# Optimization experiments

Hardware: AMD Instinct MI355X
Metric: run time of the kernel (lower is better)

The kernel has to match this reference:

```python
import jax, jax.numpy as jnp
import numpy as np

N, E, C_IN, HID, G, L = 100000, 1600000, 64, 32, 128, 3
NEG_SLOPE = 0.01  # F.leaky_relu default


def setup_inputs() -> dict:
    key = jax.random.key(0)
    ks = jax.random.split(key, 10)
    x = jax.random.normal(ks[0], (N, C_IN), dtype=jnp.float32)
    src = jax.random.randint(ks[1], (E,), 0, N, dtype=jnp.int32)
    dst = jax.random.randint(ks[2], (E,), 0, N, dtype=jnp.int32)
    batch = jnp.sort(jax.random.randint(ks[3], (N,), 0, G, dtype=jnp.int32))
    def glorot(k, fan_in, fan_out):
        lim = np.sqrt(6.0 / (fan_in + fan_out)).astype(np.float32)
        return jax.random.uniform(k, (fan_in, fan_out), jnp.float32, -lim, lim)
    W0 = glorot(ks[4], C_IN, HID); b0 = jnp.zeros((HID,), jnp.float32)
    W1 = glorot(ks[5], HID, HID);  b1 = jnp.zeros((HID,), jnp.float32)
    W2 = glorot(ks[6], HID, HID);  b2 = jnp.zeros((HID,), jnp.float32)
    return {"x": x, "W0": W0, "b0": b0, "W1": W1, "b1": b1,
            "W2": W2, "b2": b2, "src": src, "dst": dst, "batch": batch}


def _gcn_conv(x, W, b, src, dst, dinv):
    # PyG GCNConv: h = x W; aggregate with sym-norm (A + I)
    h = x @ W                                   # [N, H]
    coef = (dinv[src] * dinv[dst])[:, None]     # [E, 1]
    msg = h[src] * coef                         # gather + scale
    agg = jax.ops.segment_sum(msg, dst, num_segments=N)
    agg = agg + h * (dinv * dinv)[:, None]      # self-loop term
    return agg + b


def _mean_pool(x, batch, counts):
    s = jax.ops.segment_sum(x, batch, num_segments=G)
    return s / counts[:, None]


def reference(x, W0, b0, W1, b1, W2, b2, src, dst, batch):
    # degree with self loops (edge weight 1), as PyG gcn_norm does
    deg = jax.ops.segment_sum(jnp.ones((E,), x.dtype), dst, num_segments=N) + 1.0
    dinv = jax.lax.rsqrt(deg)
    counts = jnp.maximum(
        jax.ops.segment_sum(jnp.ones((N,), x.dtype), batch, num_segments=G), 1.0)
    params = [(W0, b0), (W1, b1), (W2, b2)]
    feats = []
    h = x
    for W, b in params:
        h = _gcn_conv(h, W, b, src, dst, dinv)
        h = jax.nn.leaky_relu(h, NEG_SLOPE)
        feats.append(_mean_pool(h, batch, counts))
    merge = jnp.mean(jnp.stack(feats, axis=0), axis=0)  # [G, HID]
    return merge
```

## Files before the change

### kernel.cpp

```cpp
#include <hip/hip_runtime.h>
#include <hip/hip_bf16.h>

#define NN 100000
#define NE 1600000
#define CIN 64
#define HIDN 32
#define NG 128
#define SLOPE 0.01f


__global__ __launch_bounds__(256) void k_rank(const int* __restrict__ dst,
                                              int* __restrict__ deg,
                                              int* __restrict__ rank,
                                              int qbase, int qcount) {
  int i0 = blockIdx.x * 256 + threadIdx.x;
  if (i0 >= qcount) return;
  int i = qbase + i0;
  int4 d = ((const int4*)dst)[i];
  int4 r;
  r.x = atomicAdd(&deg[d.x], 1);
  r.y = atomicAdd(&deg[d.y], 1);
  r.z = atomicAdd(&deg[d.z], 1);
  r.w = atomicAdd(&deg[d.w], 1);
  ((int4*)rank)[i] = r;
}


__global__ __launch_bounds__(256) void k_scan1(const int* __restrict__ deg,
                                               int* __restrict__ bsum) {
  __shared__ int s[256];
  int t = threadIdx.x;
  int base = blockIdx.x * 1024 + t * 4;
  int sum = 0;
#pragma unroll
  for (int j = 0; j < 4; ++j) {
    int idx = base + j;
    if (idx < NN) sum += deg[idx];
  }
  s[t] = sum;
  __syncthreads();
  for (int o = 128; o > 0; o >>= 1) {
    if (t < o) s[t] += s[t + o];
    __syncthreads();
  }
  if (t == 0) bsum[blockIdx.x] = s[0];
}

__global__ __launch_bounds__(256) void k_mid(int* __restrict__ bsum,
                                             int* __restrict__ rowp,
                                             const int* __restrict__ batch,
                                             float* __restrict__ cinv, int nblk) {
  __shared__ int s[128];
  __shared__ int sb[NG + 1];
  int t = threadIdx.x;
  if (t < nblk) s[t] = bsum[t];
  if (t <= NG) {
    int lo = 0, hi = NN;
    while (lo < hi) {
      int mid = (lo + hi) >> 1;
      if (batch[mid] < t) lo = mid + 1; else hi = mid;
    }
    sb[t] = lo;
  }
  __syncthreads();
  if (t == 0) {
    int run = 0;
    for (int i = 0; i < nblk; ++i) {
      int v = s[i];
      s[i] = run;
      run += v;
    }
    rowp[NN] = run;
  }
  __syncthreads();
  if (t < nblk) bsum[t] = s[t];
  if (t < NG) {
    int c = sb[t + 1] - sb[t];
    cinv[t] = 1.0f / (3.0f * fmaxf((float)c, 1.0f));
  }
}

__global__ __launch_bounds__(256) void k_scan3(const int* __restrict__ deg,
                                               const int* __restrict__ bsum,
                                               int* __restrict__ rowp,
                                               float* __restrict__ dinv) {
  __shared__ int s[256];
  int t = threadIdx.x;
  int base = blockIdx.x * 1024 + t * 4;
  int d0 = 0, d1 = 0, d2 = 0, d3 = 0;
  if (base < NN) d0 = deg[base];
  if (base + 1 < NN) d1 = deg[base + 1];
  if (base + 2 < NN) d2 = deg[base + 2];
  if (base + 3 < NN) d3 = deg[base + 3];
  int ts = d0 + d1 + d2 + d3;
  s[t] = ts;
  __syncthreads();
  for (int o = 1; o < 256; o <<= 1) {
    int v = (t >= o) ? s[t - o] : 0;
    __syncthreads();
    s[t] += v;
    __syncthreads();
  }
  int run = bsum[blockIdx.x] + s[t] - ts;
  if (base < NN) { rowp[base] = run; dinv[base] = rsqrtf((float)d0 + 1.0f); run += d0; }
  if (base + 1 < NN) { rowp[base + 1] = run; dinv[base + 1] = rsqrtf((float)d1 + 1.0f); run += d1; }
  if (base + 2 < NN) { rowp[base + 2] = run; dinv[base + 2] = rsqrtf((float)d2 + 1.0f); run += d2; }
  if (base + 3 < NN) { rowp[base + 3] = run; dinv[base + 3] = rsqrtf((float)d3 + 1.0f); run += d3; }
}

__global__ __launch_bounds__(256) void k_scatter(const int* __restrict__ src,
                                                 const int* __restrict__ dst,
                                                 const int* __restrict__ rank,
                                                 const int* __restrict__ rowp,
                                                 int* __restrict__ col,
                                                 int qbase, int qcount) {
  int i0 = blockIdx.x * 256 + threadIdx.x;
  if (i0 >= qcount) return;
  int i = qbase + i0;
  int4 d = ((const int4*)dst)[i];
  int4 r = ((const int4*)rank)[i];
  int4 s = ((const int4*)src)[i];
  col[rowp[d.x] + r.x] = s.x;
  col[rowp[d.y] + r.y] = s.y;
  col[rowp[d.z] + r.z] = s.z;
  col[rowp[d.w] + r.w] = s.w;
}


template <int K>
__global__ __launch_bounds__(256) void k_mm(const float* __restrict__ in,
                                            const float* __restrict__ W,
                                            const float* __restrict__ dinv,
                                            __hip_bfloat16* __restrict__ out) {
  __shared__ float sW[K * HIDN];
  int t = threadIdx.x;
  for (int i = t; i < K * HIDN; i += 256) sW[i] = W[i];
  __syncthreads();
  int gid = blockIdx.x * 256 + t;
  int node = gid >> 5;
  int f = gid & 31;
  if (node >= NN) return;
  const float* xr = in + node * K;
  float acc = 0.f;
#pragma unroll
  for (int k = 0; k < K; ++k) acc += xr[k] * sW[k * HIDN + f];
  out[node * HIDN + f] = __float2bfloat16(acc * dinv[node]);
}


template <int WRITE_H>
__global__ __launch_bounds__(256) void k_agg(const __hip_bfloat16* __restrict__ hs,
                                             const int* __restrict__ rowp,
                                             const int* __restrict__ col,
                                             const float* __restrict__ dinv,
                                             const int* __restrict__ batch,
                                             const float* __restrict__ cinv,
                                             const float* __restrict__ bias,
                                             float* __restrict__ hout,
                                             float* __restrict__ pool) {
  const int t = threadIdx.x;
  const int f = t & 31;
  const int sub = t >> 5;
  const float bf = bias[f];
  float pacc = 0.f;
  int gcur = -1;
  const int base = blockIdx.x * 32;
#pragma unroll
  for (int it = 0; it < 4; ++it) {
    const int i = base + it * 8 + sub;
    if (i < NN) {
      float acc = __bfloat162float(hs[i * HIDN + f]);
      const int rs = rowp[i];
      const int re = rowp[i + 1];
      int e = rs;
      for (; e + 8 <= re; e += 8) {
        const int c0 = __builtin_nontemporal_load(col + e);
        const int c1 = __builtin_nontemporal_load(col + e + 1);
        const int c2 = __builtin_nontemporal_load(col + e + 2);
        const int c3 = __builtin_nontemporal_load(col + e + 3);
        const int c4 = __builtin_nontemporal_load(col + e + 4);
        const int c5 = __builtin_nontemporal_load(col + e + 5);
        const int c6 = __builtin_nontemporal_load(col + e + 6);
        const int c7 = __builtin_nontemporal_load(col + e + 7);
        const float v0 = __bfloat162float(hs[c0 * HIDN + f]);
        const float v1 = __bfloat162float(hs[c1 * HIDN + f]);
        const float v2 = __bfloat162float(hs[c2 * HIDN + f]);
        const float v3 = __bfloat162float(hs[c3 * HIDN + f]);
        const float v4 = __bfloat162float(hs[c4 * HIDN + f]);
        const float v5 = __bfloat162float(hs[c5 * HIDN + f]);
        const float v6 = __bfloat162float(hs[c6 * HIDN + f]);
        const float v7 = __bfloat162float(hs[c7 * HIDN + f]);
        acc += ((v0 + v1) + (v2 + v3)) + ((v4 + v5) + (v6 + v7));
      }
      for (; e + 4 <= re; e += 4) {
        const int c0 = __builtin_nontemporal_load(col + e);
        const int c1 = __builtin_nontemporal_load(col + e + 1);
        const int c2 = __builtin_nontemporal_load(col + e + 2);
        const int c3 = __builtin_nontemporal_load(col + e + 3);
        const float v0 = __bfloat162float(hs[c0 * HIDN + f]);
        const float v1 = __bfloat162float(hs[c1 * HIDN + f]);
        const float v2 = __bfloat162float(hs[c2 * HIDN + f]);
        const float v3 = __bfloat162float(hs[c3 * HIDN + f]);
        acc += (v0 + v1) + (v2 + v3);
      }
      for (; e < re; ++e) acc += __bfloat162float(hs[col[e] * HIDN + f]);
      float v = acc * dinv[i] + bf;
      v = v > 0.f ? v : SLOPE * v;
      if (WRITE_H) hout[i * HIDN + f] = v;
      const int g = batch[i];
      if (g != gcur) {
        if (gcur >= 0) unsafeAtomicAdd(&pool[gcur * HIDN + f], pacc * cinv[gcur]);
        gcur = g;
        pacc = 0.f;
      }
      pacc += v;
    }
  }
  if (gcur >= 0) unsafeAtomicAdd(&pool[gcur * HIDN + f], pacc * cinv[gcur]);
}


extern "C" void kernel_launch(void* const* d_in, const int* in_sizes, int n_in,
                              void* d_out, int out_size, void* d_ws, size_t ws_size,
                              hipStream_t stream) {
  const float* x = (const float*)d_in[0];
  const float* W0 = (const float*)d_in[1];
  const float* b0 = (const float*)d_in[2];
  const float* W1 = (const float*)d_in[3];
  const float* b1 = (const float*)d_in[4];
  const float* W2 = (const float*)d_in[5];
  const float* b2 = (const float*)d_in[6];
  const int* src = (const int*)d_in[7];
  const int* dst = (const int*)d_in[8];
  const int* batch = (const int*)d_in[9];
  float* out = (float*)d_out;

  char* ws = (char*)d_ws;
  auto carve = [&](size_t bytes) -> char* {
    char* p = ws;
    ws += (bytes + 255) & ~(size_t)255;
    return p;
  };
  int* deg = (int*)carve(NN * 4);
  int* rank = (int*)carve((size_t)NE * 4);
  int* rowp = (int*)carve((NN + 1) * 4);
  int* bsum = (int*)carve(128 * 4);
  float* dinv = (float*)carve(NN * 4);
  float* cinv = (float*)carve(NG * 4);
  int* col = (int*)carve((size_t)NE * 4);
  float* hA = (float*)carve((size_t)NN * HIDN * 4);
  __hip_bfloat16* hs = (__hip_bfloat16*)carve((size_t)NN * HIDN * 2);

  hipMemsetAsync(deg, 0, NN * 4, stream);
  hipMemsetAsync(out, 0, NG * HIDN * 4, stream);

  const int QH = NE / 4 / 2;
  const int half_grid = (QH + 255) / 256;
  k_rank<<<half_grid, 256, 0, stream>>>(dst, deg, rank, 0, QH);
  k_rank<<<half_grid, 256, 0, stream>>>(dst, deg, rank, QH, QH);

  int nblk = (NN + 1023) / 1024;
  k_scan1<<<nblk, 256, 0, stream>>>(deg, bsum);
  k_mid<<<1, 256, 0, stream>>>(bsum, rowp, batch, cinv, nblk);
  k_scan3<<<nblk, 256, 0, stream>>>(deg, bsum, rowp, dinv);

  k_scatter<<<half_grid, 256, 0, stream>>>(src, dst, rank, rowp, col, 0, QH);
  k_scatter<<<half_grid, 256, 0, stream>>>(src, dst, rank, rowp, col, QH, QH);

  const int mm_grid = (NN * HIDN + 255) / 256;
  const int agg_grid = (NN + 31) / 32;

  k_mm<CIN><<<mm_grid, 256, 0, stream>>>(x, W0, dinv, hs);
  k_agg<1><<<agg_grid, 256, 0, stream>>>(hs, rowp, col, dinv, batch, cinv, b0, hA, out);
  k_mm<HIDN><<<mm_grid, 256, 0, stream>>>(hA, W1, dinv, hs);
  k_agg<1><<<agg_grid, 256, 0, stream>>>(hs, rowp, col, dinv, batch, cinv, b1, hA, out);
  k_mm<HIDN><<<mm_grid, 256, 0, stream>>>(hA, W2, dinv, hs);
  k_agg<0><<<agg_grid, 256, 0, stream>>>(hs, rowp, col, dinv, batch, cinv, b2, hA, out);
}
```

Before: 473.6 us.

## Fuse next-layer matmul into aggregation, pack ranks to bytes, merge setup kernels

Folds the next layer's dense transform into the aggregation kernel through a shared-memory tile of activations, so the fp32 hidden buffer is no longer written and read back. Edge ranks are packed into 8-bit fields, which cuts rank traffic but assumes no node gets more than 255 incoming edges. The edge-scatter and first-layer matmul share one launch, k_mid is folded into scan1/scan3, and the output memset moves into a kernel, all to reduce launch count. Bounds checks are removed on the assumption that the node count divides the block tiling evenly.

After: 439.5 us. -7.2%, faster.

```diff
diff --git a/kernel.cpp b/kernel.cpp
--- a/kernel.cpp
+++ b/kernel.cpp
@@ -7,35 +7,53 @@
 #define HIDN 32
 #define NG 128
 #define SLOPE 0.01f
+#define NBLK 98
+#define SCAT_BLOCKS 782
+#define MM0_BLOCKS 12500
+#define AGG_BLOCKS 3125
 
 
 __global__ __launch_bounds__(256) void k_rank(const int* __restrict__ dst,
                                               int* __restrict__ deg,
-                                              int* __restrict__ rank,
-                                              int qbase, int qcount) {
-  int i0 = blockIdx.x * 256 + threadIdx.x;
-  if (i0 >= qcount) return;
-  int i = qbase + i0;
-  int4 d = ((const int4*)dst)[i];
-  int4 r;
-  r.x = atomicAdd(&deg[d.x], 1);
-  r.y = atomicAdd(&deg[d.y], 1);
-  r.z = atomicAdd(&deg[d.z], 1);
-  r.w = atomicAdd(&deg[d.w], 1);
-  ((int4*)rank)[i] = r;
+                                              unsigned int* __restrict__ rank) {
+  int i = blockIdx.x * 256 + threadIdx.x;
+  if (i * 8 >= NE) return;
+  int4 a = ((const int4*)dst)[2 * i];
+  int4 b = ((const int4*)dst)[2 * i + 1];
+  unsigned int r0 = atomicAdd(&deg[a.x], 1);
+  unsigned int r1 = atomicAdd(&deg[a.y], 1);
+  unsigned int r2 = atomicAdd(&deg[a.z], 1);
+  unsigned int r3 = atomicAdd(&deg[a.w], 1);
+  unsigned int r4 = atomicAdd(&deg[b.x], 1);
+  unsigned int r5 = atomicAdd(&deg[b.y], 1);
+  unsigned int r6 = atomicAdd(&deg[b.z], 1);
+  unsigned int r7 = atomicAdd(&deg[b.w], 1);
+  uint2 packed;
+  packed.x = r0 | (r1 << 8) | (r2 << 16) | (r3 << 24);
+  packed.y = r4 | (r5 << 8) | (r6 << 16) | (r7 << 24);
+  ((uint2*)rank)[i] = packed;
 }
 
 
 __global__ __launch_bounds__(256) void k_scan1(const int* __restrict__ deg,
-                                               int* __restrict__ bsum) {
+                                               int* __restrict__ bsum,
+                                               float* __restrict__ dinv,
+                                               const int* __restrict__ batch,
+                                               float* __restrict__ cinv,
+                                               float* __restrict__ out) {
   __shared__ int s[256];
+  __shared__ int sb[NG + 1];
   int t = threadIdx.x;
   int base = blockIdx.x * 1024 + t * 4;
   int sum = 0;
 #pragma unroll
   for (int j = 0; j < 4; ++j) {
     int idx = base + j;
-    if (idx < NN) sum += deg[idx];
+    if (idx < NN) {
+      int d = deg[idx];
+      sum += d;
+      dinv[idx] = rsqrtf((float)d + 1.0f);
+    }
   }
   s[t] = sum;
   __syncthreads();
@@ -44,48 +62,32 @@
     __syncthreads();
   }
   if (t == 0) bsum[blockIdx.x] = s[0];
-}
-
-__global__ __launch_bounds__(256) void k_mid(int* __restrict__ bsum,
-                                             int* __restrict__ rowp,
-                                             const int* __restrict__ batch,
-                                             float* __restrict__ cinv, int nblk) {
-  __shared__ int s[128];
-  __shared__ int sb[NG + 1];
-  int t = threadIdx.x;
-  if (t < nblk) s[t] = bsum[t];
-  if (t <= NG) {
-    int lo = 0, hi = NN;
-    while (lo < hi) {
-      int mid = (lo + hi) >> 1;
-      if (batch[mid] < t) lo = mid + 1; else hi = mid;
-    }
-    sb[t] = lo;
-  }
-  __syncthreads();
-  if (t == 0) {
-    int run = 0;
-    for (int i = 0; i < nblk; ++i) {
-      int v = s[i];
-      s[i] = run;
-      run += v;
-    }
-    rowp[NN] = run;
-  }
-  __syncthreads();
-  if (t < nblk) bsum[t] = s[t];
-  if (t < NG) {
-    int c = sb[t + 1] - sb[t];
-    cinv[t] = 1.0f / (3.0f * fmaxf((float)c, 1.0f));
-  }
-}
+  if (blockIdx.x == 0) {
+    if (t <= NG) {
+      int lo = 0, hi = NN;
+      while (lo < hi) {
+        int mid = (lo + hi) >> 1;
+        if (batch[mid] < t) lo = mid + 1; else hi = mid;
+      }
+      sb[t] = lo;
+    }
+    for (int i = t; i < NG * HIDN; i += 256) out[i] = 0.f;
+    __syncthreads();
+    if (t < NG) {
+      int c = sb[t + 1] - sb[t];
+      cinv[t] = 1.0f / (3.0f * fmaxf((float)c, 1.0f));
+    }
+  }
+}
+
 
 __global__ __launch_bounds__(256) void k_scan3(const int* __restrict__ deg,
                                                const int* __restrict__ bsum,
-                                               int* __restrict__ rowp,
-                                               float* __restrict__ dinv) {
+                                               int* __restrict__ rowp) {
   __shared__ int s[256];
+  __shared__ int sb2[128];
   int t = threadIdx.x;
+  if (t < 128) sb2[t] = (t < NBLK) ? bsum[t] : 0;
   int base = blockIdx.x * 1024 + t * 4;
   int d0 = 0, d1 = 0, d2 = 0, d3 = 0;
   if (base < NN) d0 = deg[base];
@@ -95,60 +97,71 @@
   int ts = d0 + d1 + d2 + d3;
   s[t] = ts;
   __syncthreads();
+  for (int o = 1; o < 128; o <<= 1) {
+    int v = (t < 128 && t >= o) ? sb2[t - o] : 0;
+    __syncthreads();
+    if (t < 128) sb2[t] += v;
+    __syncthreads();
+  }
   for (int o = 1; o < 256; o <<= 1) {
     int v = (t >= o) ? s[t - o] : 0;
     __syncthreads();
     s[t] += v;
     __syncthreads();
   }
-  int run = bsum[blockIdx.x] + s[t] - ts;
-  if (base < NN) { rowp[base] = run; dinv[base] = rsqrtf((float)d0 + 1.0f); run += d0; }
-  if (base + 1 < NN) { rowp[base + 1] = run; dinv[base + 1] = rsqrtf((float)d1 + 1.0f); run += d1; }
-  if (base + 2 < NN) { rowp[base + 2] = run; dinv[base + 2] = rsqrtf((float)d2 + 1.0f); run += d2; }
-  if (base + 3 < NN) { rowp[base + 3] = run; dinv[base + 3] = rsqrtf((float)d3 + 1.0f); run += d3; }
-}
-
-__global__ __launch_bounds__(256) void k_scatter(const int* __restrict__ src,
-                                                 const int* __restrict__ dst,
-                                                 const int* __restrict__ rank,
-                                                 const int* __restrict__ rowp,
-                                                 int* __restrict__ col,
-                                                 int qbase, int qcount) {
-  int i0 = blockIdx.x * 256 + threadIdx.x;
-  if (i0 >= qcount) return;
-  int i = qbase + i0;
-  int4 d = ((const int4*)dst)[i];
-  int4 r = ((const int4*)rank)[i];
-  int4 s = ((const int4*)src)[i];
-  col[rowp[d.x] + r.x] = s.x;
-  col[rowp[d.y] + r.y] = s.y;
-  col[rowp[d.z] + r.z] = s.z;
-  col[rowp[d.w] + r.w] = s.w;
-}
-
-
-template <int K>
-__global__ __launch_bounds__(256) void k_mm(const float* __restrict__ in,
-                                            const float* __restrict__ W,
+  int blockoff = blockIdx.x ? sb2[blockIdx.x - 1] : 0;
+  int run = blockoff + s[t] - ts;
+  if (base < NN) { rowp[base] = run; run += d0; }
+  if (base + 1 < NN) { rowp[base + 1] = run; run += d1; }
+  if (base + 2 < NN) { rowp[base + 2] = run; run += d2; }
+  if (base + 3 < NN) { rowp[base + 3] = run; run += d3; }
+  if (blockIdx.x == NBLK - 1 && t == 255) rowp[NN] = run;
+}
+
+
+__global__ __launch_bounds__(256) void k_sm(const int* __restrict__ src,
+                                            const int* __restrict__ dst,
+                                            const unsigned int* __restrict__ rank,
+                                            const int* __restrict__ rowp,
+                                            int* __restrict__ col,
+                                            const float* __restrict__ x,
+                                            const float* __restrict__ W0,
                                             const float* __restrict__ dinv,
-                                            __hip_bfloat16* __restrict__ out) {
-  __shared__ float sW[K * HIDN];
+                                            __hip_bfloat16* __restrict__ hs) {
+  __shared__ float sW[CIN * HIDN];
+  if (blockIdx.x < SCAT_BLOCKS) {
+    int i = blockIdx.x * 256 + threadIdx.x;
+    if (i * 8 >= NE) return;
+    int4 da = ((const int4*)dst)[2 * i];
+    int4 db = ((const int4*)dst)[2 * i + 1];
+    uint2 rr = ((const uint2*)rank)[i];
+    int4 sa = ((const int4*)src)[2 * i];
+    int4 sb = ((const int4*)src)[2 * i + 1];
+    col[rowp[da.x] + (int)(rr.x & 0xff)] = sa.x;
+    col[rowp[da.y] + (int)((rr.x >> 8) & 0xff)] = sa.y;
+    col[rowp[da.z] + (int)((rr.x >> 16) & 0xff)] = sa.z;
+    col[rowp[da.w] + (int)(rr.x >> 24)] = sa.w;
+    col[rowp[db.x] + (int)(rr.y & 0xff)] = sb.x;
+    col[rowp[db.y] + (int)((rr.y >> 8) & 0xff)] = sb.y;
+    col[rowp[db.z] + (int)((rr.y >> 16) & 0xff)] = sb.z;
+    col[rowp[db.w] + (int)(rr.y >> 24)] = sb.w;
+    return;
+  }
   int t = threadIdx.x;
-  for (int i = t; i < K * HIDN; i += 256) sW[i] = W[i];
+  for (int i = t; i < CIN * HIDN; i += 256) sW[i] = W0[i];
   __syncthreads();
-  int gid = blockIdx.x * 256 + t;
+  int gid = (blockIdx.x - SCAT_BLOCKS) * 256 + t;
   int node = gid >> 5;
   int f = gid & 31;
-  if (node >= NN) return;
-  const float* xr = in + node * K;
+  const float* xr = x + node * CIN;
   float acc = 0.f;
 #pragma unroll
-  for (int k = 0; k < K; ++k) acc += xr[k] * sW[k * HIDN + f];
-  out[node * HIDN + f] = __float2bfloat16(acc * dinv[node]);
-}
-
-
-template <int WRITE_H>
+  for (int k = 0; k < CIN; ++k) acc += xr[k] * sW[k * HIDN + f];
+  hs[node * HIDN + f] = __float2bfloat16(acc * dinv[node]);
+}
+
+
+template <int FUSE>
 __global__ __launch_bounds__(256) void k_agg(const __hip_bfloat16* __restrict__ hs,
                                              const int* __restrict__ rowp,
                                              const int* __restrict__ col,
@@ -156,67 +169,87 @@
                                              const int* __restrict__ batch,
                                              const float* __restrict__ cinv,
                                              const float* __restrict__ bias,
-                                             float* __restrict__ hout,
+                                             const float* __restrict__ Wn,
+                                             __hip_bfloat16* __restrict__ hs_next,
                                              float* __restrict__ pool) {
+  __shared__ float vrow[32][32];
   const int t = threadIdx.x;
   const int f = t & 31;
   const int sub = t >> 5;
+  const int base = blockIdx.x * 32;
+
+  float wreg[HIDN];
+  if (FUSE) {
+#pragma unroll
+    for (int k = 0; k < HIDN; ++k) wreg[k] = Wn[k * HIDN + f];
+  }
+
   const float bf = bias[f];
   float pacc = 0.f;
   int gcur = -1;
-  const int base = blockIdx.x * 32;
 #pragma unroll
   for (int it = 0; it < 4; ++it) {
     const int i = base + it * 8 + sub;
-    if (i < NN) {
-      float acc = __bfloat162float(hs[i * HIDN + f]);
-      const int rs = rowp[i];
-      const int re = rowp[i + 1];
-      int e = rs;
-      for (; e + 8 <= re; e += 8) {
-        const int c0 = __builtin_nontemporal_load(col + e);
-        const int c1 = __builtin_nontemporal_load(col + e + 1);
-        const int c2 = __builtin_nontemporal_load(col + e + 2);
-        const int c3 = __builtin_nontemporal_load(col + e + 3);
-        const int c4 = __builtin_nontemporal_load(col + e + 4);
-        const int c5 = __builtin_nontemporal_load(col + e + 5);
-        const int c6 = __builtin_nontemporal_load(col + e + 6);
-        const int c7 = __builtin_nontemporal_load(col + e + 7);
-        const float v0 = __bfloat162float(hs[c0 * HIDN + f]);
-        const float v1 = __bfloat162float(hs[c1 * HIDN + f]);
-        const float v2 = __bfloat162float(hs[c2 * HIDN + f]);
-        const float v3 = __bfloat162float(hs[c3 * HIDN + f]);
-        const float v4 = __bfloat162float(hs[c4 * HIDN + f]);
-        const float v5 = __bfloat162float(hs[c5 * HIDN + f]);
-        const float v6 = __bfloat162float(hs[c6 * HIDN + f]);
-        const float v7 = __bfloat162float(hs[c7 * HIDN + f]);
-        acc += ((v0 + v1) + (v2 + v3)) + ((v4 + v5) + (v6 + v7));
-      }
-      for (; e + 4 <= re; e += 4) {
-        const int c0 = __builtin_nontemporal_load(col + e);
-        const int c1 = __builtin_nontemporal_load(col + e + 1);
-        const int c2 = __builtin_nontemporal_load(col + e + 2);
-        const int c3 = __builtin_nontemporal_load(col + e + 3);
-        const float v0 = __bfloat162float(hs[c0 * HIDN + f]);
-        const float v1 = __bfloat162float(hs[c1 * HIDN + f]);
-        const float v2 = __bfloat162float(hs[c2 * HIDN + f]);
-        const float v3 = __bfloat162float(hs[c3 * HIDN + f]);
-        acc += (v0 + v1) + (v2 + v3);
-      }
-      for (; e < re; ++e) acc += __bfloat162float(hs[col[e] * HIDN + f]);
-      float v = acc * dinv[i] + bf;
-      v = v > 0.f ? v : SLOPE * v;
-      if (WRITE_H) hout[i * HIDN + f] = v;
-      const int g = batch[i];
-      if (g != gcur) {
-        if (gcur >= 0) unsafeAtomicAdd(&pool[gcur * HIDN + f], pacc * cinv[gcur]);
-        gcur = g;
-        pacc = 0.f;
-      }
-      pacc += v;
-    }
+    float acc = __bfloat162float(hs[i * HIDN + f]);
+    const int rs = rowp[i];
+    const int re = rowp[i + 1];
+    int e = rs;
+    for (; e + 8 <= re; e += 8) {
+      const int c0 = __builtin_nontemporal_load(col + e);
+      const int c1 = __builtin_nontemporal_load(col + e + 1);
+      const int c2 = __builtin_nontemporal_load(col + e + 2);
+      const int c3 = __builtin_nontemporal_load(col + e + 3);
+      const int c4 = __builtin_nontemporal_load(col + e + 4);
+      const int c5 = __builtin_nontemporal_load(col + e + 5);
+      const int c6 = __builtin_nontemporal_load(col + e + 6);
+      const int c7 = __builtin_nontemporal_load(col + e + 7);
+      const float v0 = __bfloat162float(hs[c0 * HIDN + f]);
+      const float v1 = __bfloat162float(hs[c1 * HIDN + f]);
+      const float v2 = __bfloat162float(hs[c2 * HIDN + f]);
+      const float v3 = __bfloat162float(hs[c3 * HIDN + f]);
+      const float v4 = __bfloat162float(hs[c4 * HIDN + f]);
+      const float v5 = __bfloat162float(hs[c5 * HIDN + f]);
+      const float v6 = __bfloat162float(hs[c6 * HIDN + f]);
+      const float v7 = __bfloat162float(hs[c7 * HIDN + f]);
+      acc += ((v0 + v1) + (v2 + v3)) + ((v4 + v5) + (v6 + v7));
+    }
+    for (; e + 4 <= re; e += 4) {
+      const int c0 = __builtin_nontemporal_load(col + e);
+      const int c1 = __builtin_nontemporal_load(col + e + 1);
+      const int c2 = __builtin_nontemporal_load(col + e + 2);
+      const int c3 = __builtin_nontemporal_load(col + e + 3);
+      const float v0 = __bfloat162float(hs[c0 * HIDN + f]);
+      const float v1 = __bfloat162float(hs[c1 * HIDN + f]);
+      const float v2 = __bfloat162float(hs[c2 * HIDN + f]);
+      const float v3 = __bfloat162float(hs[c3 * HIDN + f]);
+      acc += (v0 + v1) + (v2 + v3);
+    }
+    for (; e < re; ++e) acc += __bfloat162float(hs[col[e] * HIDN + f]);
+    float v = acc * dinv[i] + bf;
+    v = v > 0.f ? v : SLOPE * v;
+    vrow[it * 8 + sub][f] = v;
+    const int g = batch[i];
+    if (g != gcur) {
+      if (gcur >= 0) unsafeAtomicAdd(&pool[gcur * HIDN + f], pacc * cinv[gcur]);
+      gcur = g;
+      pacc = 0.f;
+    }
+    pacc += v;
   }
   if (gcur >= 0) unsafeAtomicAdd(&pool[gcur * HIDN + f], pacc * cinv[gcur]);
+
+  if (FUSE) {
+    __syncthreads();
+#pragma unroll
+    for (int q = 0; q < 4; ++q) {
+      const int li = sub * 4 + q;
+      const int i = base + li;
+      float a = 0.f;
+#pragma unroll
+      for (int k = 0; k < HIDN; ++k) a += vrow[li][k] * wreg[k];
+      hs_next[i * HIDN + f] = __float2bfloat16(a * dinv[i]);
+    }
+  }
 }
 
 
@@ -242,38 +275,26 @@
     return p;
   };
   int* deg = (int*)carve(NN * 4);
-  int* rank = (int*)carve((size_t)NE * 4);
+  unsigned int* rank = (unsigned int*)carve((size_t)NE);
   int* rowp = (int*)carve((NN + 1) * 4);
   int* bsum = (int*)carve(128 * 4);
   float* dinv = (float*)carve(NN * 4);
   float* cinv = (float*)carve(NG * 4);
   int* col = (int*)carve((size_t)NE * 4);
-  float* hA = (float*)carve((size_t)NN * HIDN * 4);
-  __hip_bfloat16* hs = (__hip_bfloat16*)carve((size_t)NN * HIDN * 2);
+  __hip_bfloat16* hsA = (__hip_bfloat16*)carve((size_t)NN * HIDN * 2);
+  __hip_bfloat16* hsB = (__hip_bfloat16*)carve((size_t)NN * HIDN * 2);
 
   hipMemsetAsync(deg, 0, NN * 4, stream);
-  hipMemsetAsync(out, 0, NG * HIDN * 4, stream);
-
-  const int QH = NE / 4 / 2;
-  const int half_grid = (QH + 255) / 256;
-  k_rank<<<half_grid, 256, 0, stream>>>(dst, deg, rank, 0, QH);
-  k_rank<<<half_grid, 256, 0, stream>>>(dst, deg, rank, QH, QH);
-
-  int nblk = (NN + 1023) / 1024;
-  k_scan1<<<nblk, 256, 0, stream>>>(deg, bsum);
-  k_mid<<<1, 256, 0, stream>>>(bsum, rowp, batch, cinv, nblk);
-  k_scan3<<<nblk, 256, 0, stream>>>(deg, bsum, rowp, dinv);
-
-  k_scatter<<<half_grid, 256, 0, stream>>>(src, dst, rank, rowp, col, 0, QH);
-  k_scatter<<<half_grid, 256, 0, stream>>>(src, dst, rank, rowp, col, QH, QH);
-
-  const int mm_grid = (NN * HIDN + 255) / 256;
-  const int agg_grid = (NN + 31) / 32;
-
-  k_mm<CIN><<<mm_grid, 256, 0, stream>>>(x, W0, dinv, hs);
-  k_agg<1><<<agg_grid, 256, 0, stream>>>(hs, rowp, col, dinv, batch, cinv, b0, hA, out);
-  k_mm<HIDN><<<mm_grid, 256, 0, stream>>>(hA, W1, dinv, hs);
-  k_agg<1><<<agg_grid, 256, 0, stream>>>(hs, rowp, col, dinv, batch, cinv, b1, hA, out);
-  k_mm<HIDN><<<mm_grid, 256, 0, stream>>>(hA, W2, dinv, hs);
-  k_agg<0><<<agg_grid, 256, 0, stream>>>(hs, rowp, col, dinv, batch, cinv, b2, hA, out);
-}
+
+  k_rank<<<SCAT_BLOCKS, 256, 0, stream>>>(dst, deg, rank);
+  k_scan1<<<NBLK, 256, 0, stream>>>(deg, bsum, dinv, batch, cinv, out);
+  k_scan3<<<NBLK, 256, 0, stream>>>(deg, bsum, rowp);
+  k_sm<<<SCAT_BLOCKS + MM0_BLOCKS, 256, 0, stream>>>(src, dst, rank, rowp, col,
+                                                     x, W0, dinv, hsA);
+  k_agg<1><<<AGG_BLOCKS, 256, 0, stream>>>(hsA, rowp, col, dinv, batch, cinv,
+                                           b0, W1, hsB, out);
+  k_agg<1><<<AGG_BLOCKS, 256, 0, stream>>>(hsB, rowp, col, dinv, batch, cinv,
+                                           b1, W2, hsA, out);
+  k_agg<0><<<AGG_BLOCKS, 256, 0, stream>>>(hsA, rowp, col, dinv, batch, cinv,
+                                           b2, nullptr, nullptr, out);
+}
```
